# Optimization experiments

Measured on AMD Instinct MI355X. Metric: run time of the kernel, lower is better.

Reference implementation:

```python
import jax, jax.numpy as jnp
import numpy as np

B, T, IN, H, OUT = 32, 1024, 256, 768, 128


def setup_inputs() -> dict:
    key = jax.random.key(0)
    ks = jax.random.split(key, 11)
    s = 0.05
    return {
        "x": jax.random.normal(ks[0], (B, T, IN), dtype=jnp.float32),
        "W_ih0": jax.random.normal(ks[1], (4 * H, IN), dtype=jnp.float32) * s,
        "W_hh0": jax.random.normal(ks[2], (4 * H, H), dtype=jnp.float32) * s,
        "b_ih0": jax.random.normal(ks[3], (4 * H,), dtype=jnp.float32) * s,
        "b_hh0": jax.random.normal(ks[4], (4 * H,), dtype=jnp.float32) * s,
        "W_ih1": jax.random.normal(ks[5], (4 * H, H), dtype=jnp.float32) * s,
        "W_hh1": jax.random.normal(ks[6], (4 * H, H), dtype=jnp.float32) * s,
        "b_ih1": jax.random.normal(ks[7], (4 * H,), dtype=jnp.float32) * s,
        "b_hh1": jax.random.normal(ks[8], (4 * H,), dtype=jnp.float32) * s,
        "W_lin": jax.random.normal(ks[9], (OUT, H), dtype=jnp.float32) * s,
        "b_lin": jax.random.normal(ks[10], (OUT,), dtype=jnp.float32) * s,
    }


def _lstm_layer(x_btd, W_ih, W_hh, b_ih, b_hh):
    # Input-side GEMM for all timesteps at once: [B,T,4H]
    xg = jnp.einsum("btd,gd->btg", x_btd, W_ih) + b_ih + b_hh
    xg = jnp.swapaxes(xg, 0, 1)  # time-major [T,B,4H]
    h0 = jnp.zeros((x_btd.shape[0], W_hh.shape[1]), x_btd.dtype)

    def step(carry, gx):
        h, c = carry
        g = gx + h @ W_hh.T  # [B,4H]
        i, f, gg, o = jnp.split(g, 4, axis=-1)  # PyTorch gate order i,f,g,o
        i, f, o = jax.nn.sigmoid(i), jax.nn.sigmoid(f), jax.nn.sigmoid(o)
        c = f * c + i * jnp.tanh(gg)
        h = o * jnp.tanh(c)
        return (h, c), h

    _, hs = jax.lax.scan(step, (h0, h0), xg)  # hs: [T,B,H]
    return jnp.swapaxes(hs, 0, 1)  # [B,T,H]


def reference(x, W_ih0, W_hh0, b_ih0, b_hh0, W_ih1, W_hh1, b_ih1, b_hh1, W_lin, b_lin):
    h1 = _lstm_layer(x, W_ih0, W_hh0, b_ih0, b_hh0)
    h2 = _lstm_layer(h1, W_ih1, W_hh1, b_ih1, b_hh1)  # eval mode: inter-layer dropout off
    return jnp.einsum("bth,oh->bto", h2, W_lin) + b_lin
```

## Files before the change

kernel.cpp:

```cpp
#include <hip/hip_runtime.h>

#define Tt    1024
#define INF   256
#define Hh    768
#define OUTF  128

#define NWG_L0  48
#define NWG_L1  48
#define NWG_LIN 2
#define NWGC    (NWG_L0 + NWG_L1 + NWG_LIN)
#define NWG     (NWGC + 1)
#define NTHR    1024

typedef unsigned int       u32;
typedef unsigned long long u64;
typedef unsigned short     u16;
typedef __attribute__((ext_vector_type(8))) short bf16x8;
typedef __attribute__((ext_vector_type(4))) float f32x4;

#define PROG_OFF 0
#define GO_OFF   16384
#define HA_OFF   32768
#define HB_OFF   131072
#define WS_BYTES 229376
#define HPS 24576

#define ASTR_B 1552

__device__ __forceinline__ float sigf(float v){ return 1.0f/(1.0f+__expf(-v)); }
__device__ __forceinline__ u16 f2bf(float f){
    u32 u = __float_as_uint(f);
    return (u16)((u + 0x7fffu + ((u>>16)&1u)) >> 16);
}
__device__ __forceinline__ u64 ld64ws(const u16* p){
    return __hip_atomic_load((const u64*)p, __ATOMIC_RELAXED, __HIP_MEMORY_SCOPE_AGENT);
}
__device__ __forceinline__ void st32ws(u16* p, u32 v){
    __hip_atomic_store((u32*)p, v, __ATOMIC_RELAXED, __HIP_MEMORY_SCOPE_AGENT);
}
__device__ __forceinline__ u32 ldu32(const u32* p){
    return __hip_atomic_load(p, __ATOMIC_RELAXED, __HIP_MEMORY_SCOPE_AGENT);
}
__device__ __forceinline__ void stu32(u32* p, u32 v){
    __hip_atomic_store(p, v, __ATOMIC_RELAXED, __HIP_MEMORY_SCOPE_AGENT);
}

__global__ void prologue(char* ws){
    int i = blockIdx.x * 256 + threadIdx.x;
    if (i < WS_BYTES / 4) ((u32*)ws)[i] = 0u;
}

__device__ __forceinline__ bf16x8 load8w(const float* p){
    float4 v0 = *(const float4*)(p);
    float4 v1 = *(const float4*)(p + 4);
    bf16x8 r;
    r[0]=(short)f2bf(v0.x); r[1]=(short)f2bf(v0.y); r[2]=(short)f2bf(v0.z); r[3]=(short)f2bf(v0.w);
    r[4]=(short)f2bf(v1.x); r[5]=(short)f2bf(v1.y); r[6]=(short)f2bf(v1.z); r[7]=(short)f2bf(v1.w);
    return r;
}

__global__ __launch_bounds__(NTHR) void lstm_persist(
    const float* __restrict__ x,
    const float* __restrict__ Wih0, const float* __restrict__ Whh0,
    const float* __restrict__ bih0, const float* __restrict__ bhh0,
    const float* __restrict__ Wih1, const float* __restrict__ Whh1,
    const float* __restrict__ bih1, const float* __restrict__ bhh1,
    const float* __restrict__ Wlin, const float* __restrict__ blin,
    float* __restrict__ out, char* ws)
{
    u32* prog = (u32*)(ws + PROG_OFF);
    u32* gol  = (u32*)(ws + GO_OFF);
    u16* hA   = (u16*)(ws + HA_OFF);
    u16* hB   = (u16*)(ws + HB_OFF);

    const int wg  = blockIdx.x;
    const int tid = threadIdx.x;

    if (wg == NWGC) {
        for (int s = 0; s < Tt + 2; ++s) {
            if (tid < NWGC) {
                const u32 tg = (u32)(s + 1);
                while (ldu32(prog + tid * 32) < tg) __builtin_amdgcn_s_sleep(1);
            }
            __syncthreads();
            if (tid < NWGC) stu32(gol + tid * 32, (u32)(s + 1));
        }
        return;
    }

    __shared__ __align__(16) char smem[49664];
    char*  actb  = smem;
    float* red   = (float*)smem;
    float* part  = (float*)(smem + 33024);
    u16*   hpack = (u16*)(smem + 41472);

    const int lane = tid & 63, w = tid >> 6;
    const int quad = lane >> 4, nl = lane & 15;
    const int nt = w >> 2, ks = w & 3;
    const int b3 = tid >> 5, q = tid & 31;

    const int role  = (wg < NWG_L0) ? 0 : ((wg < NWG_L0 + NWG_L1) ? 1 : 2);
    const int jbase = (role == 0) ? wg * 16 : ((role == 1) ? (wg - NWG_L0) * 16 : 0);
    const int obase = (role == 2) ? (wg - NWG_L0 - NWG_L1) * 64 : 0;

    bf16x8 bfr[12];
    if (role == 0) {
        const int grow = nt * Hh + jbase + nl;
        #pragma unroll
        for (int fi = 0; fi < 8; ++fi) {
            const int c = fi >> 2, fc = fi & 3;
            const int ka = c * 512 + ks * 128 + fc * 32 + quad * 8;
            const float* p = (ka < 256) ? (Wih0 + (size_t)grow * 256 + ka)
                                        : (Whh0 + (size_t)grow * 768 + (ka - 256));
            bfr[fi] = load8w(p);
        }
    } else if (role == 1) {
        const int grow = nt * Hh + jbase + nl;
        #pragma unroll
        for (int fi = 0; fi < 12; ++fi) {
            const int c = fi / 6, fc = fi % 6;
            const int ka = c * 768 + ks * 192 + fc * 32 + quad * 8;
            const float* p = (ka < 768) ? (Wih1 + (size_t)grow * 768 + ka)
                                        : (Whh1 + (size_t)grow * 768 + (ka - 768));
            bfr[fi] = load8w(p);
        }
    } else {
        const int row = obase + nt * 16 + nl;
        #pragma unroll
        for (int fi = 0; fi < 6; ++fi) {
            const int ka = ks * 192 + fi * 32 + quad * 8;
            bfr[fi] = load8w(Wlin + (size_t)row * 768 + ka);
        }
    }

    float bs0 = 0.f, bs1 = 0.f, bs2 = 0.f, bs3 = 0.f, creg = 0.f, bl0 = 0.f, bl1 = 0.f;
    if (role < 2 && tid < 512) {
        const int jg = jbase + (tid >> 5);
        const float* bi = (role == 0) ? bih0 : bih1;
        const float* bh = (role == 0) ? bhh0 : bhh1;
        bs0 = bi[jg]        + bh[jg];
        bs1 = bi[768 + jg]  + bh[768 + jg];
        bs2 = bi[1536 + jg] + bh[1536 + jg];
        bs3 = bi[2304 + jg] + bh[2304 + jg];
    }
    if (role == 2) {
        bl0 = blin[obase + (tid >> 5)];
        bl1 = blin[obase + 32 + (tid >> 5)];
    }

    for (int s = 0; s < Tt + 2; ++s) {
        if (s > 0) {
            if (tid == 0) {
                while (ldu32(gol + wg * 32) < (u32)s) __builtin_amdgcn_s_sleep(1);
            }
            __syncthreads();
        }

        const bool active = (role == 0) ? (s < Tt)
                          : (role == 1) ? (s >= 1 && s <= Tt)
                          :               (s >= 2);

        if (active) {
            f32x4 acc0 = {0.f,0.f,0.f,0.f}, acc1 = {0.f,0.f,0.f,0.f};

            if (role == 0) {
                {
                    const float* xs = x + ((size_t)b3 * Tt + s) * INF + q * 8;
                    float4 v0 = *(const float4*)xs, v1 = *(const float4*)(xs + 4);
                    u64 lo = (u64)f2bf(v0.x) | ((u64)f2bf(v0.y)<<16) | ((u64)f2bf(v0.z)<<32) | ((u64)f2bf(v0.w)<<48);
                    u64 hi = (u64)f2bf(v1.x) | ((u64)f2bf(v1.y)<<16) | ((u64)f2bf(v1.z)<<32) | ((u64)f2bf(v1.w)<<48);
                    u64* dx = (u64*)(actb + b3 * ASTR_B + q * 16);
                    dx[0] = lo; dx[1] = hi;
                    const u16* src = hA + (size_t)((s + 1) & 1) * HPS + b3 * 768 + q * 8;
                    u64 h0 = ld64ws(src), h1 = ld64ws(src + 4);
                    u64* dh = (u64*)(actb + b3 * ASTR_B + (256 + q * 8) * 2);
                    dh[0] = h0; dh[1] = h1;
                    __syncthreads();
                    #pragma unroll
                    for (int fc = 0; fc < 4; ++fc) {
                        const int koff = ks * 128 + fc * 32 + quad * 8;
                        bf16x8 a0 = *(const bf16x8*)(actb + nl * ASTR_B + koff * 2);
                        bf16x8 a1 = *(const bf16x8*)(actb + (16 + nl) * ASTR_B + koff * 2);
                        acc0 = __builtin_amdgcn_mfma_f32_16x16x32_bf16(a0, bfr[fc], acc0, 0, 0, 0);
                        acc1 = __builtin_amdgcn_mfma_f32_16x16x32_bf16(a1, bfr[fc], acc1, 0, 0, 0);
                    }
                    __syncthreads();
                }
                {
                    const u16* base = hA + (size_t)((s + 1) & 1) * HPS + b3 * 768 + 256;
                    #pragma unroll
                    for (int p = 0; p < 2; ++p) {
                        const int k = q * 8 + 256 * p;
                        u64 h0 = ld64ws(base + k), h1 = ld64ws(base + k + 4);
                        u64* d = (u64*)(actb + b3 * ASTR_B + k * 2);
                        d[0] = h0; d[1] = h1;
                    }
                    __syncthreads();
                    #pragma unroll
                    for (int fc = 0; fc < 4; ++fc) {
                        const int koff = ks * 128 + fc * 32 + quad * 8;
                        bf16x8 a0 = *(const bf16x8*)(actb + nl * ASTR_B + koff * 2);
                        bf16x8 a1 = *(const bf16x8*)(actb + (16 + nl) * ASTR_B + koff * 2);
                        acc0 = __builtin_amdgcn_mfma_f32_16x16x32_bf16(a0, bfr[4 + fc], acc0, 0, 0, 0);
                        acc1 = __builtin_amdgcn_mfma_f32_16x16x32_bf16(a1, bfr[4 + fc], acc1, 0, 0, 0);
                    }
                    __syncthreads();
                }
            } else if (role == 1) {
                const int u = s - 1;
                #pragma unroll
                for (int c = 0; c < 2; ++c) {
                    const u16* ringp = (c == 0) ? (hA + (size_t)(u & 1) * HPS)
                                                : (hB + (size_t)((u + 1) & 1) * HPS);
                    const u16* base = ringp + b3 * 768;
                    #pragma unroll
                    for (int p = 0; p < 3; ++p) {
                        const int k = q * 8 + 256 * p;
                        u64 h0 = ld64ws(base + k), h1 = ld64ws(base + k + 4);
                        u64* d = (u64*)(actb + b3 * ASTR_B + k * 2);
                        d[0] = h0; d[1] = h1;
                    }
                    __syncthreads();
                    #pragma unroll
                    for (int fc = 0; fc < 6; ++fc) {
                        const int koff = ks * 192 + fc * 32 + quad * 8;
                        bf16x8 a0 = *(const bf16x8*)(actb + nl * ASTR_B + koff * 2);
                        bf16x8 a1 = *(const bf16x8*)(actb + (16 + nl) * ASTR_B + koff * 2);
                        acc0 = __builtin_amdgcn_mfma_f32_16x16x32_bf16(a0, bfr[c * 6 + fc], acc0, 0, 0, 0);
                        acc1 = __builtin_amdgcn_mfma_f32_16x16x32_bf16(a1, bfr[c * 6 + fc], acc1, 0, 0, 0);
                    }
                    __syncthreads();
                }
            } else {
                const u16* base = hB + (size_t)((s - 2) & 1) * HPS + b3 * 768;
                #pragma unroll
                for (int p = 0; p < 3; ++p) {
                    const int k = q * 8 + 256 * p;
                    u64 h0 = ld64ws(base + k), h1 = ld64ws(base + k + 4);
                    u64* d = (u64*)(actb + b3 * ASTR_B + k * 2);
                    d[0] = h0; d[1] = h1;
                }
                __syncthreads();
                #pragma unroll
                for (int fc = 0; fc < 6; ++fc) {
                    const int koff = ks * 192 + fc * 32 + quad * 8;
                    bf16x8 a0 = *(const bf16x8*)(actb + nl * ASTR_B + koff * 2);
                    bf16x8 a1 = *(const bf16x8*)(actb + (16 + nl) * ASTR_B + koff * 2);
                    acc0 = __builtin_amdgcn_mfma_f32_16x16x32_bf16(a0, bfr[fc], acc0, 0, 0, 0);
                    acc1 = __builtin_amdgcn_mfma_f32_16x16x32_bf16(a1, bfr[fc], acc1, 0, 0, 0);
                }
                __syncthreads();
            }

            *(f32x4*)(red + (size_t)((nt * 2 + 0) * 4 + ks) * 256 + nl * 16 + quad * 4) = acc0;
            *(f32x4*)(red + (size_t)((nt * 2 + 1) * 4 + ks) * 256 + nl * 16 + quad * 4) = acc1;
            __syncthreads();

            const int r2 = tid >> 5, bb = tid & 31;
            const int mtr = bb >> 4, mr = bb & 15;
            float s0 = 0.f, s1 = 0.f;
            {
                const int nt0 = r2 >> 4, nr0 = r2 & 15;
                const int nt1 = (r2 + 32) >> 4, nr1 = (r2 + 32) & 15;
                #pragma unroll
                for (int k2 = 0; k2 < 4; ++k2) {
                    s0 += red[(size_t)((nt0 * 2 + mtr) * 4 + k2) * 256 + nr0 * 16 + mr];
                    s1 += red[(size_t)((nt1 * 2 + mtr) * 4 + k2) * 256 + nr1 * 16 + mr];
                }
            }

            if (role == 2) {
                const int v = s - 2;
                float* o = out + ((size_t)bb * Tt + v) * OUTF + obase;
                o[r2]      = s0 + bl0;
                o[32 + r2] = s1 + bl1;
            } else {
                part[r2 * 33 + bb]        = s0;
                part[(r2 + 32) * 33 + bb] = s1;
                __syncthreads();
                if (tid < 512) {
                    const int jl = tid >> 5, b2 = tid & 31;
                    const float pi = bs0 + part[(jl)      * 33 + b2];
                    const float pf = bs1 + part[(16 + jl) * 33 + b2];
                    const float pg = bs2 + part[(32 + jl) * 33 + b2];
                    const float po = bs3 + part[(48 + jl) * 33 + b2];
                    const float ig = sigf(pi), fg = sigf(pf);
                    const float gv = tanhf(pg), og = sigf(po);
                    creg = fg * creg + ig * gv;
                    hpack[jl * 32 + b2] = f2bf(og * tanhf(creg));
                }
                __syncthreads();
                if (tid < 256) {
                    const int pp = tid >> 5, b2 = tid & 31;
                    const u32 val = (u32)hpack[(2 * pp) * 32 + b2]
                                  | ((u32)hpack[(2 * pp + 1) * 32 + b2] << 16);
                    u16* dst = (role == 0) ? (hA + (size_t)(s & 1) * HPS)
                                           : (hB + (size_t)((s - 1) & 1) * HPS);
                    st32ws(dst + b2 * 768 + jbase + 2 * pp, val);
                }
            }
        }

        __syncthreads();
        if (tid == 0) stu32(prog + wg * 32, (u32)(s + 1));
    }
}

extern "C" void kernel_launch(void* const* d_in, const int* in_sizes, int n_in,
                              void* d_out, int out_size, void* d_ws, size_t ws_size,
                              hipStream_t stream)
{
    const float* x    = (const float*)d_in[0];
    const float* Wih0 = (const float*)d_in[1];
    const float* Whh0 = (const float*)d_in[2];
    const float* bih0 = (const float*)d_in[3];
    const float* bhh0 = (const float*)d_in[4];
    const float* Wih1 = (const float*)d_in[5];
    const float* Whh1 = (const float*)d_in[6];
    const float* bih1 = (const float*)d_in[7];
    const float* bhh1 = (const float*)d_in[8];
    const float* Wlin = (const float*)d_in[9];
    const float* blin = (const float*)d_in[10];
    float* out = (float*)d_out;
    char*  ws  = (char*)d_ws;

    hipLaunchKernelGGL(prologue, dim3(224), dim3(256), 0, stream, ws);
    hipLaunchKernelGGL(lstm_persist, dim3(NWG), dim3(NTHR), 0, stream,
                       x, Wih0, Whh0, bih0, bhh0,
                       Wih1, Whh1, bih1, bhh1,
                       Wlin, blin, out, ws);
}
```

Before: 6.882 ms.

## Streamline LSTM step sync, prefetch hidden loads, and fuse gate reduction

The coordinator workgroup now polls progress flags with two wavefronts using ballot, with no per-iteration block barrier or sleep, so go-signals are released sooner. Hidden-state loads from global are issued up front into registers before the MFMA phases, overlapping their latency with compute. The reduction buffer is padded to avoid LDS bank conflicts, and the gate reduction is fused directly into the cell update, removing the intermediate partial buffer and one barrier. tanhf is replaced by an exp-based fast tanh, and spin loops gain guard counters that trade a little instruction overhead for bounded waits.

```diff
diff --git a/kernel.cpp b/kernel.cpp
--- a/kernel.cpp
+++ b/kernel.cpp
@@ -26,8 +26,16 @@
 #define HPS 24576
 
 #define ASTR_B 1552
+#define RSLAB 272
+#define RROW  17
+#define HPACK_OFF 34816
 
 __device__ __forceinline__ float sigf(float v){ return 1.0f/(1.0f+__expf(-v)); }
+__device__ __forceinline__ float tanhfast(float x){
+    const float cx = fminf(fmaxf(x, -15.f), 15.f);
+    const float e  = __expf(2.f * cx);
+    return (e - 1.f) / (e + 1.f);
+}
 __device__ __forceinline__ u16 f2bf(float f){
     u32 u = __float_as_uint(f);
     return (u16)((u + 0x7fffu + ((u>>16)&1u)) >> 16);
@@ -47,7 +55,8 @@
 
 __global__ void prologue(char* ws){
     int i = blockIdx.x * 256 + threadIdx.x;
-    if (i < WS_BYTES / 4) ((u32*)ws)[i] = 0u;
+    if (i < WS_BYTES / 4)
+        __hip_atomic_store(((u32*)ws) + i, 0u, __ATOMIC_RELAXED, __HIP_MEMORY_SCOPE_AGENT);
 }
 
 __device__ __forceinline__ bf16x8 load8w(const float* p){
@@ -76,23 +85,38 @@
     const int wg  = blockIdx.x;
     const int tid = threadIdx.x;
 
+    __shared__ __align__(16) char smem[49664];
+
     if (wg == NWGC) {
+        u32* cflag = (u32*)smem;
+        if (tid < 2) cflag[tid] = 0;
+        __syncthreads();
+        const int wv = tid >> 6;
+        if (wv >= 2) return;
+        const int lane = tid & 63;
+        const int line = wv * 64 + lane;
+        const bool valid = (line < NWGC);
         for (int s = 0; s < Tt + 2; ++s) {
-            if (tid < NWGC) {
-                const u32 tg = (u32)(s + 1);
-                while (ldu32(prog + tid * 32) < tg) __builtin_amdgcn_s_sleep(1);
+            const u32 tg = (u32)(s + 1);
+            bool mine = !valid;
+            int guard = 0;
+            while (guard < (1 << 27)) {
+                if (!mine) mine = (ldu32(prog + line * 32) >= tg);
+                if (__ballot(mine) == ~0ull) break;
+                ++guard;
             }
-            __syncthreads();
-            if (tid < NWGC) stu32(gol + tid * 32, (u32)(s + 1));
+            __hip_atomic_store(&cflag[wv], tg, __ATOMIC_RELAXED, __HIP_MEMORY_SCOPE_WORKGROUP);
+            guard = 0;
+            while (__hip_atomic_load(&cflag[1 - wv], __ATOMIC_RELAXED, __HIP_MEMORY_SCOPE_WORKGROUP) < tg
+                   && guard < (1 << 27)) ++guard;
+            if (valid) stu32(gol + line * 32, tg);
         }
         return;
     }
 
-    __shared__ __align__(16) char smem[49664];
     char*  actb  = smem;
     float* red   = (float*)smem;
-    float* part  = (float*)(smem + 33024);
-    u16*   hpack = (u16*)(smem + 41472);
+    u16*   hpack = (u16*)(smem + HPACK_OFF);
 
     const int lane = tid & 63, w = tid >> 6;
     const int quad = lane >> 4, nl = lane & 15;
@@ -151,7 +175,10 @@
     for (int s = 0; s < Tt + 2; ++s) {
         if (s > 0) {
             if (tid == 0) {
-                while (ldu32(gol + wg * 32) < (u32)s) __builtin_amdgcn_s_sleep(1);
+                int guard = 0;
+                while (ldu32(gol + wg * 32) < (u32)s && guard < (1 << 27)) {
+                    __builtin_amdgcn_s_sleep(1); ++guard;
+                }
             }
             __syncthreads();
         }
@@ -164,81 +191,105 @@
             f32x4 acc0 = {0.f,0.f,0.f,0.f}, acc1 = {0.f,0.f,0.f,0.f};
 
             if (role == 0) {
+                const float* xs = x + ((size_t)b3 * Tt + s) * INF + q * 8;
+                const float4 v0 = *(const float4*)xs;
+                const float4 v1 = *(const float4*)(xs + 4);
+                const u16* hp = hA + (size_t)((s + 1) & 1) * HPS + b3 * 768;
+                const u64 c0a = ld64ws(hp + q * 8);
+                const u64 c0b = ld64ws(hp + q * 8 + 4);
+                u64 c1r[4];
+                #pragma unroll
+                for (int p = 0; p < 2; ++p) {
+                    c1r[2*p]   = ld64ws(hp + 256 + q * 8 + 256 * p);
+                    c1r[2*p+1] = ld64ws(hp + 256 + q * 8 + 256 * p + 4);
+                }
                 {
-                    const float* xs = x + ((size_t)b3 * Tt + s) * INF + q * 8;
-                    float4 v0 = *(const float4*)xs, v1 = *(const float4*)(xs + 4);
-                    u64 lo = (u64)f2bf(v0.x) | ((u64)f2bf(v0.y)<<16) | ((u64)f2bf(v0.z)<<32) | ((u64)f2bf(v0.w)<<48);
-                    u64 hi = (u64)f2bf(v1.x) | ((u64)f2bf(v1.y)<<16) | ((u64)f2bf(v1.z)<<32) | ((u64)f2bf(v1.w)<<48);
+                    const u64 xlo = (u64)f2bf(v0.x) | ((u64)f2bf(v0.y)<<16) | ((u64)f2bf(v0.z)<<32) | ((u64)f2bf(v0.w)<<48);
+                    const u64 xhi = (u64)f2bf(v1.x) | ((u64)f2bf(v1.y)<<16) | ((u64)f2bf(v1.z)<<32) | ((u64)f2bf(v1.w)<<48);
                     u64* dx = (u64*)(actb + b3 * ASTR_B + q * 16);
-                    dx[0] = lo; dx[1] = hi;
-                    const u16* src = hA + (size_t)((s + 1) & 1) * HPS + b3 * 768 + q * 8;
-                    u64 h0 = ld64ws(src), h1 = ld64ws(src + 4);
+                    dx[0] = xlo; dx[1] = xhi;
                     u64* dh = (u64*)(actb + b3 * ASTR_B + (256 + q * 8) * 2);
-                    dh[0] = h0; dh[1] = h1;
-                    __syncthreads();
-                    #pragma unroll
-                    for (int fc = 0; fc < 4; ++fc) {
-                        const int koff = ks * 128 + fc * 32 + quad * 8;
-                        bf16x8 a0 = *(const bf16x8*)(actb + nl * ASTR_B + koff * 2);
-                        bf16x8 a1 = *(const bf16x8*)(actb + (16 + nl) * ASTR_B + koff * 2);
-                        acc0 = __builtin_amdgcn_mfma_f32_16x16x32_bf16(a0, bfr[fc], acc0, 0, 0, 0);
-                        acc1 = __builtin_amdgcn_mfma_f32_16x16x32_bf16(a1, bfr[fc], acc1, 0, 0, 0);
-                    }
-                    __syncthreads();
-                }
-                {
-                    const u16* base = hA + (size_t)((s + 1) & 1) * HPS + b3 * 768 + 256;
-                    #pragma unroll
-                    for (int p = 0; p < 2; ++p) {
-                        const int k = q * 8 + 256 * p;
-                        u64 h0 = ld64ws(base + k), h1 = ld64ws(base + k + 4);
-                        u64* d = (u64*)(actb + b3 * ASTR_B + k * 2);
-                        d[0] = h0; d[1] = h1;
-                    }
-                    __syncthreads();
-                    #pragma unroll
-                    for (int fc = 0; fc < 4; ++fc) {
-                        const int koff = ks * 128 + fc * 32 + quad * 8;
-                        bf16x8 a0 = *(const bf16x8*)(actb + nl * ASTR_B + koff * 2);
-                        bf16x8 a1 = *(const bf16x8*)(actb + (16 + nl) * ASTR_B + koff * 2);
-                        acc0 = __builtin_amdgcn_mfma_f32_16x16x32_bf16(a0, bfr[4 + fc], acc0, 0, 0, 0);
-                        acc1 = __builtin_amdgcn_mfma_f32_16x16x32_bf16(a1, bfr[4 + fc], acc1, 0, 0, 0);
-                    }
-                    __syncthreads();
-                }
+                    dh[0] = c0a; dh[1] = c0b;
+                }
+                __syncthreads();
+                #pragma unroll
+                for (int fc = 0; fc < 4; ++fc) {
+                    const int koff = ks * 128 + fc * 32 + quad * 8;
+                    bf16x8 a0 = *(const bf16x8*)(actb + nl * ASTR_B + koff * 2);
+                    bf16x8 a1 = *(const bf16x8*)(actb + (16 + nl) * ASTR_B + koff * 2);
+                    acc0 = __builtin_amdgcn_mfma_f32_16x16x32_bf16(a0, bfr[fc], acc0, 0, 0, 0);
+                    acc1 = __builtin_amdgcn_mfma_f32_16x16x32_bf16(a1, bfr[fc], acc1, 0, 0, 0);
+                }
+                __syncthreads();
+                #pragma unroll
+                for (int p = 0; p < 2; ++p) {
+                    u64* d = (u64*)(actb + b3 * ASTR_B + (q * 8 + 256 * p) * 2);
+                    d[0] = c1r[2*p]; d[1] = c1r[2*p+1];
+                }
+                __syncthreads();
+                #pragma unroll
+                for (int fc = 0; fc < 4; ++fc) {
+                    const int koff = ks * 128 + fc * 32 + quad * 8;
+                    bf16x8 a0 = *(const bf16x8*)(actb + nl * ASTR_B + koff * 2);
+                    bf16x8 a1 = *(const bf16x8*)(actb + (16 + nl) * ASTR_B + koff * 2);
+                    acc0 = __builtin_amdgcn_mfma_f32_16x16x32_bf16(a0, bfr[4 + fc], acc0, 0, 0, 0);
+                    acc1 = __builtin_amdgcn_mfma_f32_16x16x32_bf16(a1, bfr[4 + fc], acc1, 0, 0, 0);
+                }
+                __syncthreads();
             } else if (role == 1) {
                 const int u = s - 1;
-                #pragma unroll
-                for (int c = 0; c < 2; ++c) {
-                    const u16* ringp = (c == 0) ? (hA + (size_t)(u & 1) * HPS)
-                                                : (hB + (size_t)((u + 1) & 1) * HPS);
-                    const u16* base = ringp + b3 * 768;
-                    #pragma unroll
-                    for (int p = 0; p < 3; ++p) {
-                        const int k = q * 8 + 256 * p;
-                        u64 h0 = ld64ws(base + k), h1 = ld64ws(base + k + 4);
-                        u64* d = (u64*)(actb + b3 * ASTR_B + k * 2);
-                        d[0] = h0; d[1] = h1;
-                    }
-                    __syncthreads();
-                    #pragma unroll
-                    for (int fc = 0; fc < 6; ++fc) {
-                        const int koff = ks * 192 + fc * 32 + quad * 8;
-                        bf16x8 a0 = *(const bf16x8*)(actb + nl * ASTR_B + koff * 2);
-                        bf16x8 a1 = *(const bf16x8*)(actb + (16 + nl) * ASTR_B + koff * 2);
-                        acc0 = __builtin_amdgcn_mfma_f32_16x16x32_bf16(a0, bfr[c * 6 + fc], acc0, 0, 0, 0);
-                        acc1 = __builtin_amdgcn_mfma_f32_16x16x32_bf16(a1, bfr[c * 6 + fc], acc1, 0, 0, 0);
-                    }
-                    __syncthreads();
-                }
+                const u16* bA = hA + (size_t)(u & 1) * HPS + b3 * 768;
+                const u16* bB = hB + (size_t)((u + 1) & 1) * HPS + b3 * 768;
+                u64 rA[6], rB[6];
+                #pragma unroll
+                for (int p = 0; p < 3; ++p) {
+                    rA[2*p]   = ld64ws(bA + q * 8 + 256 * p);
+                    rA[2*p+1] = ld64ws(bA + q * 8 + 256 * p + 4);
+                    rB[2*p]   = ld64ws(bB + q * 8 + 256 * p);
+                    rB[2*p+1] = ld64ws(bB + q * 8 + 256 * p + 4);
+                }
+                #pragma unroll
+                for (int p = 0; p < 3; ++p) {
+                    u64* d = (u64*)(actb + b3 * ASTR_B + (q * 8 + 256 * p) * 2);
+                    d[0] = rA[2*p]; d[1] = rA[2*p+1];
+                }
+                __syncthreads();
+                #pragma unroll
+                for (int fc = 0; fc < 6; ++fc) {
+                    const int koff = ks * 192 + fc * 32 + quad * 8;
+                    bf16x8 a0 = *(const bf16x8*)(actb + nl * ASTR_B + koff * 2);
+                    bf16x8 a1 = *(const bf16x8*)(actb + (16 + nl) * ASTR_B + koff * 2);
+                    acc0 = __builtin_amdgcn_mfma_f32_16x16x32_bf16(a0, bfr[fc], acc0, 0, 0, 0);
+                    acc1 = __builtin_amdgcn_mfma_f32_16x16x32_bf16(a1, bfr[fc], acc1, 0, 0, 0);
+                }
+                __syncthreads();
+                #pragma unroll
+                for (int p = 0; p < 3; ++p) {
+                    u64* d = (u64*)(actb + b3 * ASTR_B + (q * 8 + 256 * p) * 2);
+                    d[0] = rB[2*p]; d[1] = rB[2*p+1];
+                }
+                __syncthreads();
+                #pragma unroll
+                for (int fc = 0; fc < 6; ++fc) {
+                    const int koff = ks * 192 + fc * 32 + quad * 8;
+                    bf16x8 a0 = *(const bf16x8*)(actb + nl * ASTR_B + koff * 2);
+                    bf16x8 a1 = *(const bf16x8*)(actb + (16 + nl) * ASTR_B + koff * 2);
+                    acc0 = __builtin_amdgcn_mfma_f32_16x16x32_bf16(a0, bfr[6 + fc], acc0, 0, 0, 0);
+                    acc1 = __builtin_amdgcn_mfma_f32_16x16x32_bf16(a1, bfr[6 + fc], acc1, 0, 0, 0);
+                }
+                __syncthreads();
             } else {
                 const u16* base = hB + (size_t)((s - 2) & 1) * HPS + b3 * 768;
-                #pragma unroll
-                for (int p = 0; p < 3; ++p) {
-                    const int k = q * 8 + 256 * p;
-                    u64 h0 = ld64ws(base + k), h1 = ld64ws(base + k + 4);
-                    u64* d = (u64*)(actb + b3 * ASTR_B + k * 2);
-                    d[0] = h0; d[1] = h1;
+                u64 rB[6];
+                #pragma unroll
+                for (int p = 0; p < 3; ++p) {
+                    rB[2*p]   = ld64ws(base + q * 8 + 256 * p);
+                    rB[2*p+1] = ld64ws(base + q * 8 + 256 * p + 4);
+                }
+                #pragma unroll
+                for (int p = 0; p < 3; ++p) {
+                    u64* d = (u64*)(actb + b3 * ASTR_B + (q * 8 + 256 * p) * 2);
+                    d[0] = rB[2*p]; d[1] = rB[2*p+1];
                 }
                 __syncthreads();
                 #pragma unroll
@@ -252,42 +303,42 @@
                 __syncthreads();
             }
 
-            *(f32x4*)(red + (size_t)((nt * 2 + 0) * 4 + ks) * 256 + nl * 16 + quad * 4) = acc0;
-            *(f32x4*)(red + (size_t)((nt * 2 + 1) * 4 + ks) * 256 + nl * 16 + quad * 4) = acc1;
+            *(f32x4*)(red + (size_t)((nt * 2 + 0) * 4 + ks) * RSLAB + nl * RROW + quad * 4) = acc0;
+            *(f32x4*)(red + (size_t)((nt * 2 + 1) * 4 + ks) * RSLAB + nl * RROW + quad * 4) = acc1;
             __syncthreads();
 
-            const int r2 = tid >> 5, bb = tid & 31;
-            const int mtr = bb >> 4, mr = bb & 15;
-            float s0 = 0.f, s1 = 0.f;
-            {
+            if (role == 2) {
+                const int r2 = tid >> 5, bb = tid & 31;
+                const int mtr = bb >> 4, mr = bb & 15;
                 const int nt0 = r2 >> 4, nr0 = r2 & 15;
                 const int nt1 = (r2 + 32) >> 4, nr1 = (r2 + 32) & 15;
+                float s0 = 0.f, s1 = 0.f;
                 #pragma unroll
                 for (int k2 = 0; k2 < 4; ++k2) {
-                    s0 += red[(size_t)((nt0 * 2 + mtr) * 4 + k2) * 256 + nr0 * 16 + mr];
-                    s1 += red[(size_t)((nt1 * 2 + mtr) * 4 + k2) * 256 + nr1 * 16 + mr];
-                }
-            }
-
-            if (role == 2) {
+                    s0 += red[(size_t)((nt0 * 2 + mtr) * 4 + k2) * RSLAB + nr0 * RROW + mr];
+                    s1 += red[(size_t)((nt1 * 2 + mtr) * 4 + k2) * RSLAB + nr1 * RROW + mr];
+                }
                 const int v = s - 2;
                 float* o = out + ((size_t)bb * Tt + v) * OUTF + obase;
                 o[r2]      = s0 + bl0;
                 o[32 + r2] = s1 + bl1;
             } else {
-                part[r2 * 33 + bb]        = s0;
-                part[(r2 + 32) * 33 + bb] = s1;
-                __syncthreads();
                 if (tid < 512) {
                     const int jl = tid >> 5, b2 = tid & 31;
-                    const float pi = bs0 + part[(jl)      * 33 + b2];
-                    const float pf = bs1 + part[(16 + jl) * 33 + b2];
-                    const float pg = bs2 + part[(32 + jl) * 33 + b2];
-                    const float po = bs3 + part[(48 + jl) * 33 + b2];
-                    const float ig = sigf(pi), fg = sigf(pf);
-                    const float gv = tanhf(pg), og = sigf(po);
+                    const int mt = b2 >> 4, mr = b2 & 15;
+                    float pv[4];
+                    #pragma unroll
+                    for (int g = 0; g < 4; ++g) {
+                        float t = 0.f;
+                        #pragma unroll
+                        for (int k2 = 0; k2 < 4; ++k2)
+                            t += red[(size_t)((g * 2 + mt) * 4 + k2) * RSLAB + jl * RROW + mr];
+                        pv[g] = t;
+                    }
+                    const float ig = sigf(bs0 + pv[0]), fg = sigf(bs1 + pv[1]);
+                    const float gv = tanhfast(bs2 + pv[2]), og = sigf(bs3 + pv[3]);
                     creg = fg * creg + ig * gv;
-                    hpack[jl * 32 + b2] = f2bf(og * tanhf(creg));
+                    hpack[jl * 32 + b2] = f2bf(og * tanhfast(creg));
                 }
                 __syncthreads();
                 if (tid < 256) {
```

Result: no change. 6.983 ms (+1.5%).

## Replace coordinator workgroup with decentralized dependency waits and triple-buffered hidden state

Applied to the files above, without the earlier changes.

Drops the dedicated coordinator workgroup that gated every step. Each workgroup now polls only the progress flags of the producers it depends on, using a wavefront ballot. Hidden-state rings go from double to triple buffering so producers can run a step ahead safely. The change also batches hidden-state loads into inline-asm dwordx4 loads, fuses the gate reduction with the activations (two hidden units per thread, one fewer barrier), pads the reduction buffer, and uses a fast tanh. The fast tanh and the hand-written cache-bypass loads add numerical and correctness risk.

```diff
diff --git a/kernel.cpp b/kernel.cpp
--- a/kernel.cpp
+++ b/kernel.cpp
@@ -8,8 +8,7 @@
 #define NWG_L0  48
 #define NWG_L1  48
 #define NWG_LIN 2
-#define NWGC    (NWG_L0 + NWG_L1 + NWG_LIN)
-#define NWG     (NWGC + 1)
+#define NWG     (NWG_L0 + NWG_L1 + NWG_LIN)
 #define NTHR    1024
 
 typedef unsigned int       u32;
@@ -19,22 +18,25 @@
 typedef __attribute__((ext_vector_type(4))) float f32x4;
 
 #define PROG_OFF 0
-#define GO_OFF   16384
-#define HA_OFF   32768
-#define HB_OFF   131072
-#define WS_BYTES 229376
-#define HPS 24576
+#define HA_OFF   16384
+#define HB_OFF   (HA_OFF + 3*49152)
+#define WS_BYTES (HB_OFF + 3*49152)
+#define HPS      24576
 
 #define ASTR_B 1552
+#define RSLAB  272
+#define RROW   17
 
 __device__ __forceinline__ float sigf(float v){ return 1.0f/(1.0f+__expf(-v)); }
+__device__ __forceinline__ float tanhfast(float x){
+    const float cx = fminf(fmaxf(x, -15.f), 15.f);
+    const float e  = __expf(2.f * cx);
+    return (e - 1.f) / (e + 1.f);
+}
 __device__ __forceinline__ u16 f2bf(float f){
     u32 u = __float_as_uint(f);
     return (u16)((u + 0x7fffu + ((u>>16)&1u)) >> 16);
 }
-__device__ __forceinline__ u64 ld64ws(const u16* p){
-    return __hip_atomic_load((const u64*)p, __ATOMIC_RELAXED, __HIP_MEMORY_SCOPE_AGENT);
-}
 __device__ __forceinline__ void st32ws(u16* p, u32 v){
     __hip_atomic_store((u32*)p, v, __ATOMIC_RELAXED, __HIP_MEMORY_SCOPE_AGENT);
 }
@@ -44,10 +46,49 @@
 __device__ __forceinline__ void stu32(u32* p, u32 v){
     __hip_atomic_store(p, v, __ATOMIC_RELAXED, __HIP_MEMORY_SCOPE_AGENT);
 }
+__device__ __forceinline__ void ld16x3(const u16* p0, const u16* p1, const u16* p2,
+                                       f32x4& r0, f32x4& r1, f32x4& r2){
+    asm volatile(
+        "global_load_dwordx4 %0, %3, off sc0 sc1\n\t"
+        "global_load_dwordx4 %1, %4, off sc0 sc1\n\t"
+        "global_load_dwordx4 %2, %5, off sc0 sc1\n\t"
+        "s_waitcnt vmcnt(0)"
+        : "=&v"(r0), "=&v"(r1), "=&v"(r2)
+        : "v"(p0), "v"(p1), "v"(p2)
+        : "memory");
+}
+__device__ __forceinline__ void ld16x6(const u16* p0, const u16* p1, const u16* p2,
+                                       const u16* p3, const u16* p4, const u16* p5,
+                                       f32x4& r0, f32x4& r1, f32x4& r2,
+                                       f32x4& r3, f32x4& r4, f32x4& r5){
+    asm volatile(
+        "global_load_dwordx4 %0, %6, off sc0 sc1\n\t"
+        "global_load_dwordx4 %1, %7, off sc0 sc1\n\t"
+        "global_load_dwordx4 %2, %8, off sc0 sc1\n\t"
+        "global_load_dwordx4 %3, %9, off sc0 sc1\n\t"
+        "global_load_dwordx4 %4, %10, off sc0 sc1\n\t"
+        "global_load_dwordx4 %5, %11, off sc0 sc1\n\t"
+        "s_waitcnt vmcnt(0)"
+        : "=&v"(r0), "=&v"(r1), "=&v"(r2), "=&v"(r3), "=&v"(r4), "=&v"(r5)
+        : "v"(p0), "v"(p1), "v"(p2), "v"(p3), "v"(p4), "v"(p5)
+        : "memory");
+}
+
+__device__ __forceinline__ void waitlines(u32* prog, int base, int cnt, u32 thr, int lane){
+    bool ok = (lane >= cnt);
+    int guard = 0;
+    while (guard < (1 << 24)) {
+        if (!ok) ok = (ldu32(prog + (base + lane) * 32) >= thr);
+        if (__ballot(ok) == ~0ull) break;
+        __builtin_amdgcn_s_sleep(1);
+        ++guard;
+    }
+}
 
 __global__ void prologue(char* ws){
     int i = blockIdx.x * 256 + threadIdx.x;
-    if (i < WS_BYTES / 4) ((u32*)ws)[i] = 0u;
+    if (i < WS_BYTES / 4)
+        __hip_atomic_store(((u32*)ws) + i, 0u, __ATOMIC_RELAXED, __HIP_MEMORY_SCOPE_AGENT);
 }
 
 __device__ __forceinline__ bf16x8 load8w(const float* p){
@@ -69,30 +110,15 @@
     float* __restrict__ out, char* ws)
 {
     u32* prog = (u32*)(ws + PROG_OFF);
-    u32* gol  = (u32*)(ws + GO_OFF);
     u16* hA   = (u16*)(ws + HA_OFF);
     u16* hB   = (u16*)(ws + HB_OFF);
 
     const int wg  = blockIdx.x;
     const int tid = threadIdx.x;
 
-    if (wg == NWGC) {
-        for (int s = 0; s < Tt + 2; ++s) {
-            if (tid < NWGC) {
-                const u32 tg = (u32)(s + 1);
-                while (ldu32(prog + tid * 32) < tg) __builtin_amdgcn_s_sleep(1);
-            }
-            __syncthreads();
-            if (tid < NWGC) stu32(gol + tid * 32, (u32)(s + 1));
-        }
-        return;
-    }
-
     __shared__ __align__(16) char smem[49664];
-    char*  actb  = smem;
-    float* red   = (float*)smem;
-    float* part  = (float*)(smem + 33024);
-    u16*   hpack = (u16*)(smem + 41472);
+    char*  actb = smem;
+    float* red  = (float*)smem;
 
     const int lane = tid & 63, w = tid >> 6;
     const int quad = lane >> 4, nl = lane & 15;
@@ -133,15 +159,16 @@
         }
     }
 
-    float bs0 = 0.f, bs1 = 0.f, bs2 = 0.f, bs3 = 0.f, creg = 0.f, bl0 = 0.f, bl1 = 0.f;
-    if (role < 2 && tid < 512) {
-        const int jg = jbase + (tid >> 5);
+    float ba0=0,ba1=0,ba2=0,ba3=0, bb0=0,bb1=0,bb2=0,bb3=0, creg0=0, creg1=0;
+    float bl0 = 0.f, bl1 = 0.f;
+    if (role < 2 && tid < 256) {
+        const int jg0 = jbase + 2 * (tid >> 5), jg1 = jg0 + 1;
         const float* bi = (role == 0) ? bih0 : bih1;
         const float* bh = (role == 0) ? bhh0 : bhh1;
-        bs0 = bi[jg]        + bh[jg];
-        bs1 = bi[768 + jg]  + bh[768 + jg];
-        bs2 = bi[1536 + jg] + bh[1536 + jg];
-        bs3 = bi[2304 + jg] + bh[2304 + jg];
+        ba0 = bi[jg0]        + bh[jg0];        bb0 = bi[jg1]        + bh[jg1];
+        ba1 = bi[768 + jg0]  + bh[768 + jg0];  bb1 = bi[768 + jg1]  + bh[768 + jg1];
+        ba2 = bi[1536 + jg0] + bh[1536 + jg0]; bb2 = bi[1536 + jg1] + bh[1536 + jg1];
+        ba3 = bi[2304 + jg0] + bh[2304 + jg0]; bb3 = bi[2304 + jg1] + bh[2304 + jg1];
     }
     if (role == 2) {
         bl0 = blin[obase + (tid >> 5)];
@@ -149,155 +176,177 @@
     }
 
     for (int s = 0; s < Tt + 2; ++s) {
-        if (s > 0) {
-            if (tid == 0) {
-                while (ldu32(gol + wg * 32) < (u32)s) __builtin_amdgcn_s_sleep(1);
-            }
-            __syncthreads();
-        }
-
         const bool active = (role == 0) ? (s < Tt)
                           : (role == 1) ? (s >= 1 && s <= Tt)
                           :               (s >= 2);
+        const int par_wA = s % 3;
+        const int par_rA = (s + 2) % 3;
+        const int par_wB = (s + 2) % 3;
+        const int par_rB = (s + 1) % 3;
+
+        if (active && w == 0) {
+            if (role == 0) {
+                if (s >= 1) waitlines(prog, 0, 48, (u32)s, lane);
+                if (s >= 2) waitlines(prog, 48, 48, (u32)(s - 1), lane);
+            } else if (role == 1) {
+                waitlines(prog, 48, 48, (u32)s, lane);
+                {
+                    const u32 thr2 = (lane < 48) ? (u32)s : (u32)(s - 1);
+                    const int idx  = (lane < 48) ? lane : (96 + (lane - 48));
+                    bool ok = (lane >= 50);
+                    int guard = 0;
+                    while (guard < (1 << 24)) {
+                        if (!ok) ok = (ldu32(prog + idx * 32) >= thr2);
+                        if (__ballot(ok) == ~0ull) break;
+                        __builtin_amdgcn_s_sleep(1);
+                        ++guard;
+                    }
+                }
+            } else {
+                waitlines(prog, 48, 48, (u32)s, lane);
+            }
+        }
+        __syncthreads();
 
         if (active) {
             f32x4 acc0 = {0.f,0.f,0.f,0.f}, acc1 = {0.f,0.f,0.f,0.f};
 
             if (role == 0) {
+                const float* xs = x + ((size_t)b3 * Tt + s) * INF + q * 8;
+                const float4 v0 = *(const float4*)xs;
+                const float4 v1 = *(const float4*)(xs + 4);
+                const u16* hp = hA + (size_t)par_rA * HPS + b3 * 768;
+                f32x4 h0, h1, h2;
+                ld16x3(hp + q * 8, hp + 256 + q * 8, hp + 512 + q * 8, h0, h1, h2);
                 {
-                    const float* xs = x + ((size_t)b3 * Tt + s) * INF + q * 8;
-                    float4 v0 = *(const float4*)xs, v1 = *(const float4*)(xs + 4);
-                    u64 lo = (u64)f2bf(v0.x) | ((u64)f2bf(v0.y)<<16) | ((u64)f2bf(v0.z)<<32) | ((u64)f2bf(v0.w)<<48);
-                    u64 hi = (u64)f2bf(v1.x) | ((u64)f2bf(v1.y)<<16) | ((u64)f2bf(v1.z)<<32) | ((u64)f2bf(v1.w)<<48);
-                    u64* dx = (u64*)(actb + b3 * ASTR_B + q * 16);
-                    dx[0] = lo; dx[1] = hi;
-                    const u16* src = hA + (size_t)((s + 1) & 1) * HPS + b3 * 768 + q * 8;
-                    u64 h0 = ld64ws(src), h1 = ld64ws(src + 4);
-                    u64* dh = (u64*)(actb + b3 * ASTR_B + (256 + q * 8) * 2);
-                    dh[0] = h0; dh[1] = h1;
-                    __syncthreads();
-                    #pragma unroll
-                    for (int fc = 0; fc < 4; ++fc) {
-                        const int koff = ks * 128 + fc * 32 + quad * 8;
-                        bf16x8 a0 = *(const bf16x8*)(actb + nl * ASTR_B + koff * 2);
-                        bf16x8 a1 = *(const bf16x8*)(actb + (16 + nl) * ASTR_B + koff * 2);
-                        acc0 = __builtin_amdgcn_mfma_f32_16x16x32_bf16(a0, bfr[fc], acc0, 0, 0, 0);
-                        acc1 = __builtin_amdgcn_mfma_f32_16x16x32_bf16(a1, bfr[fc], acc1, 0, 0, 0);
-                    }
-                    __syncthreads();
-                }
-                {
-                    const u16* base = hA + (size_t)((s + 1) & 1) * HPS + b3 * 768 + 256;
-                    #pragma unroll
-                    for (int p = 0; p < 2; ++p) {
-                        const int k = q * 8 + 256 * p;
-                        u64 h0 = ld64ws(base + k), h1 = ld64ws(base + k + 4);
-                        u64* d = (u64*)(actb + b3 * ASTR_B + k * 2);
-                        d[0] = h0; d[1] = h1;
-                    }
-                    __syncthreads();
-                    #pragma unroll
-                    for (int fc = 0; fc < 4; ++fc) {
-                        const int koff = ks * 128 + fc * 32 + quad * 8;
-                        bf16x8 a0 = *(const bf16x8*)(actb + nl * ASTR_B + koff * 2);
-                        bf16x8 a1 = *(const bf16x8*)(actb + (16 + nl) * ASTR_B + koff * 2);
-                        acc0 = __builtin_amdgcn_mfma_f32_16x16x32_bf16(a0, bfr[4 + fc], acc0, 0, 0, 0);
-                        acc1 = __builtin_amdgcn_mfma_f32_16x16x32_bf16(a1, bfr[4 + fc], acc1, 0, 0, 0);
-                    }
-                    __syncthreads();
-                }
-            } else if (role == 1) {
-                const int u = s - 1;
-                #pragma unroll
-                for (int c = 0; c < 2; ++c) {
-                    const u16* ringp = (c == 0) ? (hA + (size_t)(u & 1) * HPS)
-                                                : (hB + (size_t)((u + 1) & 1) * HPS);
-                    const u16* base = ringp + b3 * 768;
-                    #pragma unroll
-                    for (int p = 0; p < 3; ++p) {
-                        const int k = q * 8 + 256 * p;
-                        u64 h0 = ld64ws(base + k), h1 = ld64ws(base + k + 4);
-                        u64* d = (u64*)(actb + b3 * ASTR_B + k * 2);
-                        d[0] = h0; d[1] = h1;
-                    }
-                    __syncthreads();
-                    #pragma unroll
-                    for (int fc = 0; fc < 6; ++fc) {
-                        const int koff = ks * 192 + fc * 32 + quad * 8;
-                        bf16x8 a0 = *(const bf16x8*)(actb + nl * ASTR_B + koff * 2);
-                        bf16x8 a1 = *(const bf16x8*)(actb + (16 + nl) * ASTR_B + koff * 2);
-                        acc0 = __builtin_amdgcn_mfma_f32_16x16x32_bf16(a0, bfr[c * 6 + fc], acc0, 0, 0, 0);
-                        acc1 = __builtin_amdgcn_mfma_f32_16x16x32_bf16(a1, bfr[c * 6 + fc], acc1, 0, 0, 0);
-                    }
-                    __syncthreads();
-                }
-            } else {
-                const u16* base = hB + (size_t)((s - 2) & 1) * HPS + b3 * 768;
-                #pragma unroll
-                for (int p = 0; p < 3; ++p) {
-                    const int k = q * 8 + 256 * p;
-                    u64 h0 = ld64ws(base + k), h1 = ld64ws(base + k + 4);
-                    u64* d = (u64*)(actb + b3 * ASTR_B + k * 2);
-                    d[0] = h0; d[1] = h1;
-                }
-                __syncthreads();
-                #pragma unroll
-                for (int fc = 0; fc < 6; ++fc) {
-                    const int koff = ks * 192 + fc * 32 + quad * 8;
+                    uint4 xv;
+                    xv.x = (u32)f2bf(v0.x) | ((u32)f2bf(v0.y) << 16);
+                    xv.y = (u32)f2bf(v0.z) | ((u32)f2bf(v0.w) << 16);
+                    xv.z = (u32)f2bf(v1.x) | ((u32)f2bf(v1.y) << 16);
+                    xv.w = (u32)f2bf(v1.z) | ((u32)f2bf(v1.w) << 16);
+                    *(uint4*)(actb + b3 * ASTR_B + q * 16) = xv;
+                    *(f32x4*)(actb + b3 * ASTR_B + 512 + q * 16) = h0;
+                }
+                __syncthreads();
+                #pragma unroll
+                for (int fc = 0; fc < 4; ++fc) {
+                    const int koff = ks * 128 + fc * 32 + quad * 8;
                     bf16x8 a0 = *(const bf16x8*)(actb + nl * ASTR_B + koff * 2);
                     bf16x8 a1 = *(const bf16x8*)(actb + (16 + nl) * ASTR_B + koff * 2);
                     acc0 = __builtin_amdgcn_mfma_f32_16x16x32_bf16(a0, bfr[fc], acc0, 0, 0, 0);
                     acc1 = __builtin_amdgcn_mfma_f32_16x16x32_bf16(a1, bfr[fc], acc1, 0, 0, 0);
                 }
                 __syncthreads();
+                *(f32x4*)(actb + b3 * ASTR_B + q * 16)       = h1;
+                *(f32x4*)(actb + b3 * ASTR_B + 512 + q * 16) = h2;
+                __syncthreads();
+                #pragma unroll
+                for (int fc = 0; fc < 4; ++fc) {
+                    const int koff = ks * 128 + fc * 32 + quad * 8;
+                    bf16x8 a0 = *(const bf16x8*)(actb + nl * ASTR_B + koff * 2);
+                    bf16x8 a1 = *(const bf16x8*)(actb + (16 + nl) * ASTR_B + koff * 2);
+                    acc0 = __builtin_amdgcn_mfma_f32_16x16x32_bf16(a0, bfr[4 + fc], acc0, 0, 0, 0);
+                    acc1 = __builtin_amdgcn_mfma_f32_16x16x32_bf16(a1, bfr[4 + fc], acc1, 0, 0, 0);
+                }
+                __syncthreads();
+            } else if (role == 1) {
+                const u16* pA = hA + (size_t)par_rA * HPS + b3 * 768;
+                const u16* pB = hB + (size_t)par_rB * HPS + b3 * 768;
+                f32x4 a0, a1, a2, bq0, bq1, bq2;
+                ld16x6(pA + q * 8, pA + 256 + q * 8, pA + 512 + q * 8,
+                       pB + q * 8, pB + 256 + q * 8, pB + 512 + q * 8,
+                       a0, a1, a2, bq0, bq1, bq2);
+                *(f32x4*)(actb + b3 * ASTR_B + q * 16)        = a0;
+                *(f32x4*)(actb + b3 * ASTR_B + 512 + q * 16)  = a1;
+                *(f32x4*)(actb + b3 * ASTR_B + 1024 + q * 16) = a2;
+                __syncthreads();
+                #pragma unroll
+                for (int fc = 0; fc < 6; ++fc) {
+                    const int koff = ks * 192 + fc * 32 + quad * 8;
+                    bf16x8 f0 = *(const bf16x8*)(actb + nl * ASTR_B + koff * 2);
+                    bf16x8 f1 = *(const bf16x8*)(actb + (16 + nl) * ASTR_B + koff * 2);
+                    acc0 = __builtin_amdgcn_mfma_f32_16x16x32_bf16(f0, bfr[fc], acc0, 0, 0, 0);
+                    acc1 = __builtin_amdgcn_mfma_f32_16x16x32_bf16(f1, bfr[fc], acc1, 0, 0, 0);
+                }
+                __syncthreads();
+                *(f32x4*)(actb + b3 * ASTR_B + q * 16)        = bq0;
+                *(f32x4*)(actb + b3 * ASTR_B + 512 + q * 16)  = bq1;
+                *(f32x4*)(actb + b3 * ASTR_B + 1024 + q * 16) = bq2;
+                __syncthreads();
+                #pragma unroll
+                for (int fc = 0; fc < 6; ++fc) {
+                    const int koff = ks * 192 + fc * 32 + quad * 8;
+                    bf16x8 f0 = *(const bf16x8*)(actb + nl * ASTR_B + koff * 2);
+                    bf16x8 f1 = *(const bf16x8*)(actb + (16 + nl) * ASTR_B + koff * 2);
+                    acc0 = __builtin_amdgcn_mfma_f32_16x16x32_bf16(f0, bfr[6 + fc], acc0, 0, 0, 0);
+                    acc1 = __builtin_amdgcn_mfma_f32_16x16x32_bf16(f1, bfr[6 + fc], acc1, 0, 0, 0);
+                }
+                __syncthreads();
+            } else {
+                const u16* pB = hB + (size_t)par_rB * HPS + b3 * 768;
+                f32x4 bq0, bq1, bq2;
+                ld16x3(pB + q * 8, pB + 256 + q * 8, pB + 512 + q * 8, bq0, bq1, bq2);
+                *(f32x4*)(actb + b3 * ASTR_B + q * 16)        = bq0;
+                *(f32x4*)(actb + b3 * ASTR_B + 512 + q * 16)  = bq1;
+                *(f32x4*)(actb + b3 * ASTR_B + 1024 + q * 16) = bq2;
+                __syncthreads();
+                #pragma unroll
+                for (int fc = 0; fc < 6; ++fc) {
+                    const int koff = ks * 192 + fc * 32 + quad * 8;
+                    bf16x8 f0 = *(const bf16x8*)(actb + nl * ASTR_B + koff * 2);
+                    bf16x8 f1 = *(const bf16x8*)(actb + (16 + nl) * ASTR_B + koff * 2);
+                    acc0 = __builtin_amdgcn_mfma_f32_16x16x32_bf16(f0, bfr[fc], acc0, 0, 0, 0);
+                    acc1 = __builtin_amdgcn_mfma_f32_16x16x32_bf16(f1, bfr[fc], acc1, 0, 0, 0);
+                }
+                __syncthreads();
             }
 
-            *(f32x4*)(red + (size_t)((nt * 2 + 0) * 4 + ks) * 256 + nl * 16 + quad * 4) = acc0;
-            *(f32x4*)(red + (size_t)((nt * 2 + 1) * 4 + ks) * 256 + nl * 16 + quad * 4) = acc1;
+            *(f32x4*)(red + (size_t)((nt * 2 + 0) * 4 + ks) * RSLAB + nl * RROW + quad * 4) = acc0;
+            *(f32x4*)(red + (size_t)((nt * 2 + 1) * 4 + ks) * RSLAB + nl * RROW + quad * 4) = acc1;
             __syncthreads();
 
-            const int r2 = tid >> 5, bb = tid & 31;
-            const int mtr = bb >> 4, mr = bb & 15;
-            float s0 = 0.f, s1 = 0.f;
-            {
+            if (role == 2) {
+                const int r2 = tid >> 5, bb = tid & 31;
+                const int mtr = bb >> 4, mr = bb & 15;
                 const int nt0 = r2 >> 4, nr0 = r2 & 15;
                 const int nt1 = (r2 + 32) >> 4, nr1 = (r2 + 32) & 15;
+                float s0 = 0.f, s1 = 0.f;
                 #pragma unroll
                 for (int k2 = 0; k2 < 4; ++k2) {
-                    s0 += red[(size_t)((nt0 * 2 + mtr) * 4 + k2) * 256 + nr0 * 16 + mr];
-                    s1 += red[(size_t)((nt1 * 2 + mtr) * 4 + k2) * 256 + nr1 * 16 + mr];
-                }
-            }
-
-            if (role == 2) {
+                    s0 += red[(size_t)((nt0 * 2 + mtr) * 4 + k2) * RSLAB + nr0 * RROW + mr];
+                    s1 += red[(size_t)((nt1 * 2 + mtr) * 4 + k2) * RSLAB + nr1 * RROW + mr];
+                }
                 const int v = s - 2;
                 float* o = out + ((size_t)bb * Tt + v) * OUTF + obase;
                 o[r2]      = s0 + bl0;
                 o[32 + r2] = s1 + bl1;
-            } else {
-                part[r2 * 33 + bb]        = s0;
-                part[(r2 + 32) * 33 + bb] = s1;
-                __syncthreads();
-                if (tid < 512) {
-                    const int jl = tid >> 5, b2 = tid & 31;
-                    const float pi = bs0 + part[(jl)      * 33 + b2];
-                    const float pf = bs1 + part[(16 + jl) * 33 + b2];
-                    const float pg = bs2 + part[(32 + jl) * 33 + b2];
-                    const float po = bs3 + part[(48 + jl) * 33 + b2];
-                    const float ig = sigf(pi), fg = sigf(pf);
-                    const float gv = tanhf(pg), og = sigf(po);
-                    creg = fg * creg + ig * gv;
-                    hpack[jl * 32 + b2] = f2bf(og * tanhf(creg));
-                }
-                __syncthreads();
-                if (tid < 256) {
-                    const int pp = tid >> 5, b2 = tid & 31;
-                    const u32 val = (u32)hpack[(2 * pp) * 32 + b2]
-                                  | ((u32)hpack[(2 * pp + 1) * 32 + b2] << 16);
-                    u16* dst = (role == 0) ? (hA + (size_t)(s & 1) * HPS)
-                                           : (hB + (size_t)((s - 1) & 1) * HPS);
-                    st32ws(dst + b2 * 768 + jbase + 2 * pp, val);
-                }
+            } else if (tid < 256) {
+                const int jj = tid >> 5, b2 = tid & 31;
+                const int mt = b2 >> 4, mr = b2 & 15;
+                const int j0 = 2 * jj, j1 = 2 * jj + 1;
+                float p0a=0,p1a=0,p2a=0,p3a=0, p0b=0,p1b=0,p2b=0,p3b=0;
+                #pragma unroll
+                for (int k2 = 0; k2 < 4; ++k2) {
+                    p0a += red[(size_t)((0 * 2 + mt) * 4 + k2) * RSLAB + j0 * RROW + mr];
+                    p1a += red[(size_t)((1 * 2 + mt) * 4 + k2) * RSLAB + j0 * RROW + mr];
+                    p2a += red[(size_t)((2 * 2 + mt) * 4 + k2) * RSLAB + j0 * RROW + mr];
+                    p3a += red[(size_t)((3 * 2 + mt) * 4 + k2) * RSLAB + j0 * RROW + mr];
+                    p0b += red[(size_t)((0 * 2 + mt) * 4 + k2) * RSLAB + j1 * RROW + mr];
+                    p1b += red[(size_t)((1 * 2 + mt) * 4 + k2) * RSLAB + j1 * RROW + mr];
+                    p2b += red[(size_t)((2 * 2 + mt) * 4 + k2) * RSLAB + j1 * RROW + mr];
+                    p3b += red[(size_t)((3 * 2 + mt) * 4 + k2) * RSLAB + j1 * RROW + mr];
+                }
+                const float ig0 = sigf(ba0 + p0a), fg0 = sigf(ba1 + p1a);
+                const float gv0 = tanhfast(ba2 + p2a), og0 = sigf(ba3 + p3a);
+                creg0 = fg0 * creg0 + ig0 * gv0;
+                const float h0 = og0 * tanhfast(creg0);
+                const float ig1 = sigf(bb0 + p0b), fg1 = sigf(bb1 + p1b);
+                const float gv1 = tanhfast(bb2 + p2b), og1 = sigf(bb3 + p3b);
+                creg1 = fg1 * creg1 + ig1 * gv1;
+                const float h1 = og1 * tanhfast(creg1);
+                u16* dst = (role == 0) ? (hA + (size_t)par_wA * HPS)
+                                       : (hB + (size_t)par_wB * HPS);
+                st32ws(dst + b2 * 768 + jbase + j0, (u32)f2bf(h0) | ((u32)f2bf(h1) << 16));
             }
         }
 
@@ -324,7 +373,7 @@
     float* out = (float*)d_out;
     char*  ws  = (char*)d_ws;
 
-    hipLaunchKernelGGL(prologue, dim3(224), dim3(256), 0, stream, ws);
+    hipLaunchKernelGGL(prologue, dim3(304), dim3(256), 0, stream, ws);
     hipLaunchKernelGGL(lstm_persist, dim3(NWG), dim3(NTHR), 0, stream,
                        x, Wih0, Whh0, bih0, bhh0,
                        Wih1, Whh1, bih1, bhh1,
```

New measurement: 6.247 ms. 1.1x faster.
